# Optimization experiments

Hardware: AMD Instinct MI355X
Metric: run time of the kernel (lower is better)

Reference implementation:

```python
import jax, jax.numpy as jnp
import numpy as np

HID = 2048 * 3  # infl_ratio = 3
EPS = 1e-5
P_DROP = 0.5


def sign_ste(x):
    # straight-through binarization: sign in fwd, identity in bwd
    return x + jax.lax.stop_gradient(jnp.sign(x) - x)


def batchnorm(x, g, b):
    # training-mode BatchNorm1d: batch stats, biased variance
    m = jnp.mean(x, axis=0)
    v = jnp.mean((x - m) ** 2, axis=0)
    return g * (x - m) / jnp.sqrt(v + EPS) + b


def hardtanh(x):
    return jnp.clip(x, -1.0, 1.0)


def dropout(x, u):
    # u ~ U[0,1); keep where u >= p, scale by 1/(1-p)
    return jnp.where(u >= P_DROP, x / (1.0 - P_DROP), 0.0)


def setup_inputs() -> dict:
    key = jax.random.key(0)
    ks = jax.random.split(key, 16)
    B = 512
    d = {}
    d['x'] = jax.random.normal(ks[0], (B, 784), dtype=jnp.float32)
    d['drop_mask_bin'] = jax.random.uniform(ks[1], (B, HID), dtype=jnp.float32)
    d['drop_mask_real'] = jax.random.uniform(ks[2], (B, HID), dtype=jnp.float32)
    s1 = 1.0 / np.sqrt(784)
    sh = 1.0 / np.sqrt(HID)
    d['w1'] = jax.random.uniform(ks[3], (HID, 784), jnp.float32, -s1, s1)
    d['b1'] = jax.random.uniform(ks[4], (HID,), jnp.float32, -s1, s1)
    d['w2'] = jax.random.uniform(ks[5], (HID, HID), jnp.float32, -sh, sh)
    d['b2'] = jax.random.uniform(ks[6], (HID,), jnp.float32, -sh, sh)
    d['w3'] = jax.random.uniform(ks[7], (HID, HID), jnp.float32, -sh, sh)
    d['b3'] = jax.random.uniform(ks[8], (HID,), jnp.float32, -sh, sh)
    d['w4'] = jax.random.uniform(ks[9], (10, HID), jnp.float32, -sh, sh)
    d['b4'] = jax.random.uniform(ks[10], (10,), jnp.float32, -sh, sh)
    for i, k in zip((1, 2, 3), (ks[11], ks[12], ks[13])):
        d[f'g{i}'] = jnp.ones((HID,), jnp.float32)
        d[f'be{i}'] = jnp.zeros((HID,), jnp.float32)
    return d


def reference(x, drop_mask_bin, drop_mask_real, w1, b1, w2, b2, w3, b3, w4, b4,
              g1, be1, g2, be2, g3, be3):
    sg = jax.lax.stop_gradient
    # layer 1: input dim 784 -> input NOT binarized; weights binarized
    Bout1 = x @ sign_ste(w1).T + b1
    Rout1 = sg(x @ w1.T + b1)
    Bout1 = hardtanh(batchnorm(Bout1, g1, be1))
    Rout1 = sg(hardtanh(batchnorm(Rout1, g1, be1)))
    # layer 2: binarize activations and weights on binary path
    Bout2 = sign_ste(Bout1) @ sign_ste(w2).T + b2
    Rout2 = sg(Rout1 @ w2.T + b2)
    Bout2 = hardtanh(batchnorm(Bout2, g2, be2))
    Rout2 = sg(hardtanh(batchnorm(Rout2, g2, be2)))
    # layer 3 + dropout
    Bout3 = sign_ste(Bout2) @ sign_ste(w3).T + b3
    Rout3 = sg(Rout2 @ w3.T + b3)
    Bout3 = hardtanh(batchnorm(dropout(Bout3, drop_mask_bin), g3, be3))
    Rout3 = sg(hardtanh(batchnorm(dropout(Rout3, drop_mask_real), g3, be3)))
    # classifier (real-valued Linear)
    out = Bout3 @ w4.T + b4
    logp = jax.nn.log_softmax(out, axis=1)
    return (logp, out, Bout1, Rout1, Bout2, Rout2, Bout3, Rout3)
```

## Files before the change

kernel.cpp:

```cpp
#include <hip/hip_runtime.h>


typedef _Float16 f16x8 __attribute__((ext_vector_type(8)));
typedef _Float16 f16x4 __attribute__((ext_vector_type(4)));
typedef float f32x4 __attribute__((ext_vector_type(4)));
typedef int i32x4 __attribute__((ext_vector_type(4)));

#define MFMA16(a, b, c) __builtin_amdgcn_mfma_f32_16x16x32_f16((a), (b), (c), 0, 0, 0)
#define MFMAI8K64(a, b, c) __builtin_amdgcn_mfma_i32_16x16x64_i8((a), (b), (c), 0, 0, 0)

#define HIDC 6144
#define BATCH 512

#define OFF_XH    0ull
#define OFF_A8S1  851968ull
#define OFF_SB8   13434880ull
#define OFF_RF    16580608ull
#define OFF_STATS 22872064ull
#define OFF_PPART 23068672ull
#define OFF_ZPB   24641536ull
#define OFF_ZPR   37224448ull
#define OFF_ZPR2  49807360ull
#define OFF_ZPR3  62390272ull
#define OFF_W1V   74973184ull
#define OFF_WV    85196800ull
#define OFF_WS8   160694272ull
#define WS_NEED   198443008ull

#define A8_STRIDE 458752ull

__device__ __forceinline__ void load_lds16(const void* g, char* lds) {
  __builtin_amdgcn_global_load_lds((const __attribute__((address_space(1))) void*)g,
                                   (__attribute__((address_space(3))) void*)lds, 16, 0, 0);
}

__global__ __launch_bounds__(256) void k_prep_all(const float* __restrict__ x,
                                                  const float* __restrict__ w,
                                                  char* __restrict__ a8,
                                                  _Float16* __restrict__ xh,
                                                  char* __restrict__ s1,
                                                  _Float16* __restrict__ w1v) {
  if (blockIdx.x < 1792) {
    int idx = blockIdx.x * 256 + threadIdx.x;
    if (idx >= 512 * 896) return;
    int row = idx / 896, k = idx - row * 896;
    float v = (k < 784) ? x[(size_t)row * 784 + k] : 0.f;
    int q = (int)lrintf(v * 16777216.0f);
    int d0 = ((q + 128) & 255) - 128; q = (q - d0) >> 8;
    int d1 = ((q + 128) & 255) - 128; q = (q - d1) >> 8;
    int d2 = ((q + 128) & 255) - 128; q = (q - d2) >> 8;
    a8[idx] = (char)d0;
    a8[A8_STRIDE + idx] = (char)d1;
    a8[2 * A8_STRIDE + idx] = (char)d2;
    a8[3 * A8_STRIDE + idx] = (char)q;
    if (k < 832) xh[(size_t)row * 832 + k] = (_Float16)v;
  } else {
    int idx = (blockIdx.x - 1792) * 256 + threadIdx.x;
    if (idx >= 6144 * 896) return;
    int r = idx / 896, k = idx - r * 896;
    float v = (k < 784) ? w[(size_t)r * 784 + k] : 0.f;
    s1[idx] = v > 0.f ? 1 : (v < 0.f ? -1 : 0);
    if (k < 832) w1v[(size_t)r * 832 + k] = (_Float16)v;
  }
}

__global__ __launch_bounds__(256) void k_conv_w23(const float* __restrict__ w,
                                                  _Float16* __restrict__ wv,
                                                  char* __restrict__ ws8) {
  int idx = blockIdx.x * 256 + threadIdx.x;
  size_t o8 = (size_t)idx * 8;
  const float* s = w + o8;
  float4 v0 = *(const float4*)s;
  float4 v1 = *(const float4*)(s + 4);
  float a[8] = {v0.x, v0.y, v0.z, v0.w, v1.x, v1.y, v1.z, v1.w};
  f16x8 hv;
  unsigned long long sbits = 0;
#pragma unroll
  for (int e = 0; e < 8; ++e) {
    hv[e] = (_Float16)a[e];
    char sg = a[e] > 0.f ? 1 : (a[e] < 0.f ? -1 : 0);
    sbits |= ((unsigned long long)(unsigned char)sg) << (8 * e);
  }
  *(f16x8*)(wv + o8) = hv;
  *(unsigned long long*)(ws8 + o8) = sbits;
}

struct MixJob {
  const void* A;
  const void* B;
  float* C;
  int K;
  int kstart;
  int ksteps;
  int is8;
};
struct Mix6 { MixJob j[6]; };

__global__ __launch_bounds__(256) void k_gemm_mix(Mix6 P) {
  __shared__ __align__(16) char smem[65536];
  MixJob J = P.j[0];
  if (blockIdx.z == 1) J = P.j[1];
  if (blockIdx.z == 2) J = P.j[2];
  if (blockIdx.z == 3) J = P.j[3];
  if (blockIdx.z == 4) J = P.j[4];
  if (blockIdx.z == 5) J = P.j[5];
  const int t = threadIdx.x;
  const int lane = t & 63, wid = t >> 6;
  const int wm = wid >> 1, wn = wid & 1;
  const int bn = blockIdx.x, bm = blockIdx.y;
  const size_t K = (size_t)J.K;
  const int nt = J.ksteps;

  if (J.is8) {
    const char* A = (const char*)J.A;
    const char* B = (const char*)J.B;
    i32x4 acc[4][4];
#pragma unroll
    for (int mf = 0; mf < 4; ++mf)
#pragma unroll
      for (int nf = 0; nf < 4; ++nf) acc[mf][nf] = (i32x4){0, 0, 0, 0};

    auto stage = [&](char* dst, int k0) {
#pragma unroll
      for (int i = 0; i < 4; ++i) {
        int p = i * 256 + t;
        int r = p >> 3, c = p & 7;
        int cs = c ^ (r & 7);
        load_lds16(A + (size_t)(bm * 128 + r) * K + k0 + cs * 16, dst + p * 16);
      }
#pragma unroll
      for (int i = 0; i < 4; ++i) {
        int p = i * 256 + t;
        int r = p >> 3, c = p & 7;
        int cs = c ^ (r & 7);
        load_lds16(B + (size_t)(bn * 128 + r) * K + k0 + cs * 16, dst + 16384 + p * 16);
      }
    };

    stage(smem, J.kstart);
    for (int kt = 0; kt < nt; ++kt) {
      char* cbuf = smem + (kt & 1) * 32768;
      char* nbuf = smem + ((kt + 1) & 1) * 32768;
      if (kt + 1 < nt) {
        stage(nbuf, J.kstart + (kt + 1) * 128);
        asm volatile("s_waitcnt vmcnt(8)" ::: "memory");
      } else {
        asm volatile("s_waitcnt vmcnt(0)" ::: "memory");
      }
      __builtin_amdgcn_s_barrier();
      __builtin_amdgcn_s_setprio(1);
#pragma unroll
      for (int kk = 0; kk < 2; ++kk) {
        i32x4 av[4], bv[4];
#pragma unroll
        for (int mf = 0; mf < 4; ++mf) {
          int r = wm * 64 + mf * 16 + (lane & 15);
          int bo = (r * 128 + kk * 64 + (lane >> 4) * 16) ^ ((r & 7) << 4);
          av[mf] = *(const i32x4*)(cbuf + bo);
        }
#pragma unroll
        for (int nf = 0; nf < 4; ++nf) {
          int r = wn * 64 + nf * 16 + (lane & 15);
          int bo = (r * 128 + kk * 64 + (lane >> 4) * 16) ^ ((r & 7) << 4);
          bv[nf] = *(const i32x4*)(cbuf + 16384 + bo);
        }
#pragma unroll
        for (int mf = 0; mf < 4; ++mf)
#pragma unroll
          for (int nf = 0; nf < 4; ++nf) acc[mf][nf] = MFMAI8K64(av[mf], bv[nf], acc[mf][nf]);
      }
      __builtin_amdgcn_s_setprio(0);
      __builtin_amdgcn_s_barrier();
    }
#pragma unroll
    for (int mf = 0; mf < 4; ++mf)
#pragma unroll
      for (int nf = 0; nf < 4; ++nf) {
        int col = bn * 128 + wn * 64 + nf * 16 + (lane & 15);
        int row0 = bm * 128 + wm * 64 + mf * 16 + ((lane >> 4) << 2);
#pragma unroll
        for (int rr = 0; rr < 4; ++rr) {
          J.C[(size_t)(row0 + rr) * HIDC + col] = (float)acc[mf][nf][rr];
        }
      }
  } else {
    const _Float16* A = (const _Float16*)J.A;
    const _Float16* B = (const _Float16*)J.B;
    f32x4 acc[4][4];
#pragma unroll
    for (int mf = 0; mf < 4; ++mf)
#pragma unroll
      for (int nf = 0; nf < 4; ++nf) acc[mf][nf] = (f32x4){0.f, 0.f, 0.f, 0.f};

    auto stage = [&](char* dst, int k0) {
#pragma unroll
      for (int i = 0; i < 4; ++i) {
        int p = i * 256 + t;
        int r = p >> 3, c = p & 7;
        int cs = c ^ (r & 7);
        load_lds16(A + (size_t)(bm * 128 + r) * K + k0 + cs * 8, dst + p * 16);
      }
#pragma unroll
      for (int i = 0; i < 4; ++i) {
        int p = i * 256 + t;
        int r = p >> 3, c = p & 7;
        int cs = c ^ (r & 7);
        load_lds16(B + (size_t)(bn * 128 + r) * K + k0 + cs * 8, dst + 16384 + p * 16);
      }
    };

    stage(smem, J.kstart);
    for (int kt = 0; kt < nt; ++kt) {
      char* cbuf = smem + (kt & 1) * 32768;
      char* nbuf = smem + ((kt + 1) & 1) * 32768;
      if (kt + 1 < nt) {
        stage(nbuf, J.kstart + (kt + 1) * 64);
        asm volatile("s_waitcnt vmcnt(8)" ::: "memory");
      } else {
        asm volatile("s_waitcnt vmcnt(0)" ::: "memory");
      }
      __builtin_amdgcn_s_barrier();
      __builtin_amdgcn_s_setprio(1);
#pragma unroll
      for (int kk = 0; kk < 2; ++kk) {
        f16x8 av[4], bv[4];
#pragma unroll
        for (int mf = 0; mf < 4; ++mf) {
          int r = wm * 64 + mf * 16 + (lane & 15);
          int bo = (r * 128 + kk * 64 + (lane >> 4) * 16) ^ ((r & 7) << 4);
          av[mf] = *(const f16x8*)(cbuf + bo);
        }
#pragma unroll
        for (int nf = 0; nf < 4; ++nf) {
          int r = wn * 64 + nf * 16 + (lane & 15);
          int bo = (r * 128 + kk * 64 + (lane >> 4) * 16) ^ ((r & 7) << 4);
          bv[nf] = *(const f16x8*)(cbuf + 16384 + bo);
        }
#pragma unroll
        for (int mf = 0; mf < 4; ++mf)
#pragma unroll
          for (int nf = 0; nf < 4; ++nf) acc[mf][nf] = MFMA16(av[mf], bv[nf], acc[mf][nf]);
      }
      __builtin_amdgcn_s_setprio(0);
      __builtin_amdgcn_s_barrier();
    }
#pragma unroll
    for (int mf = 0; mf < 4; ++mf)
#pragma unroll
      for (int nf = 0; nf < 4; ++nf) {
        int col = bn * 128 + wn * 64 + nf * 16 + (lane & 15);
        int row0 = bm * 128 + wm * 64 + mf * 16 + ((lane >> 4) << 2);
#pragma unroll
        for (int rr = 0; rr < 4; ++rr) {
          J.C[(size_t)(row0 + rr) * HIDC + col] = acc[mf][nf][rr];
        }
      }
  }
}

struct StJob { const float* Z; const float* Zp0; const float* Zp1; const float* Zp2;
               const float* msk; int digitmode; };
struct St2 { StJob j[2]; const float* bias; int dodrop; double* ppart; };

__global__ __launch_bounds__(256) void k_stats_part(St2 P) {
  __shared__ double sm[4][64];
  __shared__ double sq[4][64];
  const int z = blockIdx.z;
  StJob J = z ? P.j[1] : P.j[0];
  const int li = threadIdx.x & 63, rg = threadIdx.x >> 6;
  const int col = blockIdx.x * 64 + li;
  const double bb = P.dodrop ? (double)P.bias[col] : 0.0;
  double s = 0.0, s2 = 0.0;
#pragma unroll 4
  for (int rr = 0; rr < 16; ++rr) {
    int r = blockIdx.y * 64 + rg * 16 + rr;
    size_t i = (size_t)r * HIDC + col;
    double v;
    if (J.digitmode) {
      double d0 = (double)J.Z[i], d1 = (double)J.Zp0[i];
      double d2 = (double)J.Zp1[i], d3 = (double)J.Zp2[i];
      v = (((d3 * 256.0 + d2) * 256.0 + d1) * 256.0 + d0) * (1.0 / 16777216.0);
    } else {
      v = (double)J.Z[i];
      if (J.Zp0) v += (double)J.Zp0[i];
      if (J.Zp1) v += (double)J.Zp1[i];
      if (J.Zp2) v += (double)J.Zp2[i];
    }
    if (P.dodrop) v = (J.msk[i] >= 0.5f) ? 2.0 * (v + bb) : 0.0;
    s += v;
    s2 += v * v;
  }
  sm[rg][li] = s;
  sq[rg][li] = s2;
  __syncthreads();
  if (rg == 0) {
    double S = sm[0][li] + sm[1][li] + sm[2][li] + sm[3][li];
    double S2 = sq[0][li] + sq[1][li] + sq[2][li] + sq[3][li];
    size_t o = ((size_t)(z * 8 + blockIdx.y) * 2) * HIDC + col;
    P.ppart[o] = S;
    P.ppart[o + HIDC] = S2;
  }
}

__global__ __launch_bounds__(256) void k_stats_fin(const double* __restrict__ ppart,
                                                   double* __restrict__ stats) {
  const int z = blockIdx.z;
  const int c = blockIdx.x * 256 + threadIdx.x;
  double S = 0.0, S2 = 0.0;
#pragma unroll
  for (int y = 0; y < 8; ++y) {
    size_t o = ((size_t)(z * 8 + y) * 2) * HIDC + c;
    S += ppart[o];
    S2 += ppart[o + HIDC];
  }
  double m = S / 512.0;
  double var = S2 / 512.0 - m * m;
  stats[z * 2 * HIDC + c] = m;
  stats[z * 2 * HIDC + HIDC + c] = 1.0 / sqrt(var + 1e-5);
}

struct BnJob { float* Z; const float* Zp0; const float* Zp1; const float* Zp2;
               const float* Zp3; void* aux; const float* msk; int auxmode; int digitmode; };
struct Bn2 {
  BnJob j[2];
  const double* stats;
  const float* g; const float* be; const float* bias;
  int dodrop;
};

__global__ __launch_bounds__(256) void k_bn2(Bn2 P) {
  const int z = blockIdx.z;
  BnJob J = z ? P.j[1] : P.j[0];
  const double* m_arr = P.stats + (size_t)z * 2 * HIDC;
  const double* r_arr = m_arr + HIDC;
  int idx = blockIdx.x * 256 + threadIdx.x;
  int row = idx / 1536;
  int c4 = (idx - row * 1536) * 4;
  size_t base = (size_t)row * HIDC + c4;
  double vv[4];
  if (J.digitmode) {
    float4 d0 = *(const float4*)(J.Zp0 + base);
    float4 d1 = *(const float4*)(J.Zp1 + base);
    float4 d2 = *(const float4*)(J.Zp2 + base);
    float4 d3 = *(const float4*)(J.Zp3 + base);
    const float* p0 = &d0.x;
    const float* p1 = &d1.x;
    const float* p2 = &d2.x;
    const float* p3 = &d3.x;
#pragma unroll
    for (int e = 0; e < 4; ++e)
      vv[e] = ((((double)p3[e] * 256.0 + (double)p2[e]) * 256.0 + (double)p1[e]) * 256.0 +
               (double)p0[e]) * (1.0 / 16777216.0);
  } else {
    float4 zv = *(const float4*)(J.Z + base);
    vv[0] = zv.x; vv[1] = zv.y; vv[2] = zv.z; vv[3] = zv.w;
    if (J.Zp0) {
      float4 t4 = *(const float4*)(J.Zp0 + base);
      vv[0] += t4.x; vv[1] += t4.y; vv[2] += t4.z; vv[3] += t4.w;
    }
    if (J.Zp1) {
      float4 t4 = *(const float4*)(J.Zp1 + base);
      vv[0] += t4.x; vv[1] += t4.y; vv[2] += t4.z; vv[3] += t4.w;
    }
    if (J.Zp2) {
      float4 t4 = *(const float4*)(J.Zp2 + base);
      vv[0] += t4.x; vv[1] += t4.y; vv[2] += t4.z; vv[3] += t4.w;
    }
  }
  float mk[4] = {1.f, 1.f, 1.f, 1.f};
  if (P.dodrop) {
    float4 t4 = *(const float4*)(J.msk + base);
    mk[0] = t4.x; mk[1] = t4.y; mk[2] = t4.z; mk[3] = t4.w;
  }
  float o[4];
  f16x4 a4;
  int sbits = 0;
#pragma unroll
  for (int e = 0; e < 4; ++e) {
    int c = c4 + e;
    double v = vv[e];
    if (P.dodrop) v = (mk[e] >= 0.5f) ? 2.0 * (v + (double)P.bias[c]) : 0.0;
    double bnv = (double)P.g[c] * ((v - m_arr[c]) * r_arr[c]) + (double)P.be[c];
    bnv = bnv > 1.0 ? 1.0 : (bnv < -1.0 ? -1.0 : bnv);
    o[e] = (float)bnv;
    char sg = bnv > 0.0 ? 1 : (bnv < 0.0 ? -1 : 0);
    sbits |= ((int)(unsigned char)sg) << (8 * e);
    a4[e] = (_Float16)o[e];
  }
  float4 ov = {o[0], o[1], o[2], o[3]};
  *(float4*)(J.Z + base) = ov;
  if (J.auxmode == 0) *(int*)((char*)J.aux + base) = sbits;
  if (J.auxmode == 1) *(f16x4*)((_Float16*)J.aux + base) = a4;
}

__global__ __launch_bounds__(256) void k_head(const float* __restrict__ B3,
                                              const float* __restrict__ w4,
                                              const float* __restrict__ b4,
                                              float* __restrict__ out,
                                              float* __restrict__ logp) {
  const int row = blockIdx.x, t = threadIdx.x;
  float acc[10];
#pragma unroll
  for (int j = 0; j < 10; ++j) acc[j] = 0.f;
  const float* a = B3 + (size_t)row * HIDC;
  for (int k4 = t; k4 < 1536; k4 += 256) {
    float4 av = *(const float4*)(a + k4 * 4);
#pragma unroll
    for (int j = 0; j < 10; ++j) {
      float4 wv = *(const float4*)(w4 + (size_t)j * HIDC + k4 * 4);
      acc[j] += av.x * wv.x + av.y * wv.y + av.z * wv.z + av.w * wv.w;
    }
  }
#pragma unroll
  for (int j = 0; j < 10; ++j)
    for (int off = 32; off; off >>= 1) acc[j] += __shfl_down(acc[j], off);
  __shared__ float sred[4][10];
  int wid = t >> 6, ln = t & 63;
  if (ln == 0)
#pragma unroll
    for (int j = 0; j < 10; ++j) sred[wid][j] = acc[j];
  __syncthreads();
  if (t == 0) {
    double o[10];
    double mx = -1e300;
#pragma unroll
    for (int j = 0; j < 10; ++j) {
      o[j] = (double)sred[0][j] + sred[1][j] + sred[2][j] + sred[3][j] + (double)b4[j];
      mx = o[j] > mx ? o[j] : mx;
    }
    double s = 0.0;
#pragma unroll
    for (int j = 0; j < 10; ++j) s += exp(o[j] - mx);
    double l = log(s) + mx;
#pragma unroll
    for (int j = 0; j < 10; ++j) {
      out[row * 10 + j] = (float)o[j];
      logp[row * 10 + j] = (float)(o[j] - l);
    }
  }
}

extern "C" void kernel_launch(void* const* d_in, const int* in_sizes, int n_in,
                              void* d_out, int out_size, void* d_ws, size_t ws_size,
                              hipStream_t stream) {
  const float* x   = (const float*)d_in[0];
  const float* mkb = (const float*)d_in[1];
  const float* mkr = (const float*)d_in[2];
  const float* w1  = (const float*)d_in[3];
  const float* w2  = (const float*)d_in[5];
  const float* w3  = (const float*)d_in[7];
  const float* b3  = (const float*)d_in[8];
  const float* w4  = (const float*)d_in[9];
  const float* b4  = (const float*)d_in[10];
  const float* g1  = (const float*)d_in[11]; const float* be1 = (const float*)d_in[12];
  const float* g2  = (const float*)d_in[13]; const float* be2 = (const float*)d_in[14];
  const float* g3  = (const float*)d_in[15]; const float* be3 = (const float*)d_in[16];

  float* outp = (float*)d_out;
  float* logp = outp;
  float* outo = outp + 5120;
  float* B1 = outp + 10240;
  float* R1 = outp + 3155968;
  float* B2 = outp + 6301696;
  float* R2 = outp + 9447424;
  float* B3 = outp + 12593152;
  float* R3 = outp + 15738880;

  char* ws = (char*)d_ws;
  _Float16* xh  = (_Float16*)(ws + OFF_XH);
  char* a8      = (char*)(ws + OFF_A8S1);
  char* s1      = (char*)(ws + OFF_A8S1 + 4ull * A8_STRIDE);
  char* sB8     = (char*)(ws + OFF_SB8);
  _Float16* rF  = (_Float16*)(ws + OFF_RF);
  double* stats = (double*)(ws + OFF_STATS);
  double* ppart = (double*)(ws + OFF_PPART);
  float* zpb    = (float*)(ws + OFF_ZPB);
  float* zpr    = (float*)(ws + OFF_ZPR);
  float* zpr2   = (float*)(ws + OFF_ZPR2);
  float* zpr3   = (float*)(ws + OFF_ZPR3);
  _Float16* w1v = (_Float16*)(ws + OFF_W1V);
  _Float16* wv  = (_Float16*)(ws + OFF_WV);
  char* ws8     = (char*)(ws + OFF_WS8);

  k_prep_all<<<23296, 256, 0, stream>>>(x, w1, a8, xh, s1, w1v);
  {
    Mix6 P{};
    P.j[0] = {a8,                 s1, zpb,  896, 0, 7, 1};
    P.j[1] = {a8 + A8_STRIDE,     s1, zpr,  896, 0, 7, 1};
    P.j[2] = {a8 + 2 * A8_STRIDE, s1, zpr2, 896, 0, 7, 1};
    P.j[3] = {a8 + 3 * A8_STRIDE, s1, zpr3, 896, 0, 7, 1};
    P.j[4] = {xh, w1v, R1, 832, 0, 13, 0};
    P.j[5] = P.j[4];
    k_gemm_mix<<<dim3(48, 4, 5), 256, 0, stream>>>(P);
  }
  {
    St2 S{};
    S.j[0] = {zpb, zpr, zpr2, zpr3, nullptr, 1};
    S.j[1] = {R1, nullptr, nullptr, nullptr, nullptr, 0};
    S.bias = nullptr; S.dodrop = 0; S.ppart = ppart;
    k_stats_part<<<dim3(96, 8, 2), 256, 0, stream>>>(S);
    k_stats_fin<<<dim3(24, 1, 2), 256, 0, stream>>>(ppart, stats);
    Bn2 B{};
    B.j[0] = {B1, zpb, zpr, zpr2, zpr3, sB8, nullptr, 0, 1};
    B.j[1] = {R1, nullptr, nullptr, nullptr, nullptr, rF, nullptr, 1, 0};
    B.stats = stats; B.g = g1; B.be = be1; B.bias = nullptr; B.dodrop = 0;
    k_bn2<<<dim3(3072, 1, 2), 256, 0, stream>>>(B);
  }
  k_conv_w23<<<18432, 256, 0, stream>>>(w2, wv, ws8);
  {
    Mix6 P{};
    P.j[0] = {sB8, ws8, B2,  HIDC, 0,    24, 1};
    P.j[1] = {sB8, ws8, zpb, HIDC, 3072, 24, 1};
    P.j[2] = {rF,  wv,  R2,  HIDC, 0,    48, 0};
    P.j[3] = {rF,  wv,  zpr, HIDC, 3072, 48, 0};
    k_gemm_mix<<<dim3(48, 4, 4), 256, 0, stream>>>(P);
  }
  {
    St2 S{};
    S.j[0] = {B2, zpb, nullptr, nullptr, nullptr, 0};
    S.j[1] = {R2, zpr, nullptr, nullptr, nullptr, 0};
    S.bias = nullptr; S.dodrop = 0; S.ppart = ppart;
    k_stats_part<<<dim3(96, 8, 2), 256, 0, stream>>>(S);
    k_stats_fin<<<dim3(24, 1, 2), 256, 0, stream>>>(ppart, stats);
    Bn2 B{};
    B.j[0] = {B2, zpb, nullptr, nullptr, nullptr, sB8, nullptr, 0, 0};
    B.j[1] = {R2, zpr, nullptr, nullptr, nullptr, rF, nullptr, 1, 0};
    B.stats = stats; B.g = g2; B.be = be2; B.bias = nullptr; B.dodrop = 0;
    k_bn2<<<dim3(3072, 1, 2), 256, 0, stream>>>(B);
  }
  k_conv_w23<<<18432, 256, 0, stream>>>(w3, wv, ws8);
  {
    Mix6 P{};
    P.j[0] = {sB8, ws8, B3,  HIDC, 0,    24, 1};
    P.j[1] = {sB8, ws8, zpb, HIDC, 3072, 24, 1};
    P.j[2] = {rF,  wv,  R3,  HIDC, 0,    48, 0};
    P.j[3] = {rF,  wv,  zpr, HIDC, 3072, 48, 0};
    k_gemm_mix<<<dim3(48, 4, 4), 256, 0, stream>>>(P);
  }
  {
    St2 S{};
    S.j[0] = {B3, zpb, nullptr, nullptr, mkb, 0};
    S.j[1] = {R3, zpr, nullptr, nullptr, mkr, 0};
    S.bias = b3; S.dodrop = 1; S.ppart = ppart;
    k_stats_part<<<dim3(96, 8, 2), 256, 0, stream>>>(S);
    k_stats_fin<<<dim3(24, 1, 2), 256, 0, stream>>>(ppart, stats);
    Bn2 B{};
    B.j[0] = {B3, zpb, nullptr, nullptr, nullptr, nullptr, mkb, 2, 0};
    B.j[1] = {R3, zpr, nullptr, nullptr, nullptr, nullptr, mkr, 2, 0};
    B.stats = stats; B.g = g3; B.be = be3; B.bias = b3; B.dodrop = 1;
    k_bn2<<<dim3(3072, 1, 2), 256, 0, stream>>>(B);
  }
  k_head<<<512, 256, 0, stream>>>(B3, w4, b4, outo, logp);
}
```

Before: 454.3 us.

## Fuse BatchNorm column statistics into GEMM epilogue and drop split-K for layers 2-3

Layers 2 and 3 no longer split K into two halves with partial outputs. Each GEMM block now covers the full K range and writes the final output directly. Its epilogue also accumulates per-column sum and sum-of-squares in double, applying the dropout mask and bias for layer 3, reduces them across waves through LDS and writes per-block partials. A small finalize kernel combines the four row-block partials, which removes the separate stats pass, its re-read of the GEMM outputs, and the split-K partial reads and writes. The trade-off is a grid halved to 384 blocks with twice-longer K loops, which lowers parallelism, plus extra epilogue work and mask loads inside the GEMM.

```diff
diff --git a/kernel.cpp b/kernel.cpp
--- a/kernel.cpp
+++ b/kernel.cpp
@@ -89,12 +89,16 @@
   const void* A;
   const void* B;
   float* C;
+  const float* msk;
+  const float* bias;
   int K;
   int kstart;
   int ksteps;
   int is8;
+  int slot;
+  int dodrop;
 };
-struct Mix6 { MixJob j[6]; };
+struct Mix6 { MixJob j[6]; double* ppart; };
 
 __global__ __launch_bounds__(256) void k_gemm_mix(Mix6 P) {
   __shared__ __align__(16) char smem[65536];
@@ -111,6 +115,10 @@
   const size_t K = (size_t)J.K;
   const int nt = J.ksteps;
 
+  double s[4], s2[4];
+#pragma unroll
+  for (int nf = 0; nf < 4; ++nf) { s[nf] = 0.0; s2[nf] = 0.0; }
+
   if (J.is8) {
     const char* A = (const char*)J.A;
     const char* B = (const char*)J.B;
@@ -183,6 +191,25 @@
           J.C[(size_t)(row0 + rr) * HIDC + col] = (float)acc[mf][nf][rr];
         }
       }
+    if (J.slot >= 0) {
+#pragma unroll
+      for (int mf = 0; mf < 4; ++mf)
+#pragma unroll
+        for (int nf = 0; nf < 4; ++nf) {
+          int col = bn * 128 + wn * 64 + nf * 16 + (lane & 15);
+          int row0 = bm * 128 + wm * 64 + mf * 16 + ((lane >> 4) << 2);
+#pragma unroll
+          for (int rr = 0; rr < 4; ++rr) {
+            double v = (double)acc[mf][nf][rr];
+            if (J.dodrop) {
+              float mv = J.msk[(size_t)(row0 + rr) * HIDC + col];
+              v = (mv >= 0.5f) ? 2.0 * (v + (double)J.bias[col]) : 0.0;
+            }
+            s[nf] += v;
+            s2[nf] += v * v;
+          }
+        }
+    }
   } else {
     const _Float16* A = (const _Float16*)J.A;
     const _Float16* B = (const _Float16*)J.B;
@@ -255,6 +282,60 @@
           J.C[(size_t)(row0 + rr) * HIDC + col] = acc[mf][nf][rr];
         }
       }
+    if (J.slot >= 0) {
+#pragma unroll
+      for (int mf = 0; mf < 4; ++mf)
+#pragma unroll
+        for (int nf = 0; nf < 4; ++nf) {
+          int col = bn * 128 + wn * 64 + nf * 16 + (lane & 15);
+          int row0 = bm * 128 + wm * 64 + mf * 16 + ((lane >> 4) << 2);
+#pragma unroll
+          for (int rr = 0; rr < 4; ++rr) {
+            double v = (double)acc[mf][nf][rr];
+            if (J.dodrop) {
+              float mv = J.msk[(size_t)(row0 + rr) * HIDC + col];
+              v = (mv >= 0.5f) ? 2.0 * (v + (double)J.bias[col]) : 0.0;
+            }
+            s[nf] += v;
+            s2[nf] += v * v;
+          }
+        }
+    }
+  }
+
+  if (J.slot >= 0) {
+#pragma unroll
+    for (int nf = 0; nf < 4; ++nf) {
+      s[nf] += __shfl_xor(s[nf], 16);
+      s[nf] += __shfl_xor(s[nf], 32);
+      s2[nf] += __shfl_xor(s2[nf], 16);
+      s2[nf] += __shfl_xor(s2[nf], 32);
+    }
+    __syncthreads();
+    double* sred = (double*)smem;
+    if ((lane >> 4) == 0) {
+#pragma unroll
+      for (int nf = 0; nf < 4; ++nf) {
+        int ix = (((wm * 2 + wn) * 4 + nf) * 16 + (lane & 15)) * 2;
+        sred[ix] = s[nf];
+        sred[ix + 1] = s2[nf];
+      }
+    }
+    __syncthreads();
+    if (wm == 0 && (lane >> 4) == 0) {
+#pragma unroll
+      for (int nf = 0; nf < 4; ++nf) {
+        int l = lane & 15;
+        int i0 = (((0 * 2 + wn) * 4 + nf) * 16 + l) * 2;
+        int i1 = (((1 * 2 + wn) * 4 + nf) * 16 + l) * 2;
+        double S = sred[i0] + sred[i1];
+        double S2 = sred[i0 + 1] + sred[i1 + 1];
+        int col = bn * 128 + wn * 64 + nf * 16 + l;
+        size_t o = ((size_t)(J.slot * 4 + bm) * 2) * HIDC + col;
+        P.ppart[o] = S;
+        P.ppart[o + HIDC] = S2;
+      }
+    }
   }
 }
 
@@ -319,6 +400,23 @@
   stats[z * 2 * HIDC + HIDC + c] = 1.0 / sqrt(var + 1e-5);
 }
 
+__global__ __launch_bounds__(256) void k_stats_fin4(const double* __restrict__ ppart,
+                                                    double* __restrict__ stats) {
+  const int z = blockIdx.z;
+  const int c = blockIdx.x * 256 + threadIdx.x;
+  double S = 0.0, S2 = 0.0;
+#pragma unroll
+  for (int b = 0; b < 4; ++b) {
+    size_t o = ((size_t)(z * 4 + b) * 2) * HIDC + c;
+    S += ppart[o];
+    S2 += ppart[o + HIDC];
+  }
+  double m = S / 512.0;
+  double var = S2 / 512.0 - m * m;
+  stats[z * 2 * HIDC + c] = m;
+  stats[z * 2 * HIDC + HIDC + c] = 1.0 / sqrt(var + 1e-5);
+}
+
 struct BnJob { float* Z; const float* Zp0; const float* Zp1; const float* Zp2;
                const float* Zp3; void* aux; const float* msk; int auxmode; int digitmode; };
 struct Bn2 {
@@ -358,14 +456,6 @@
       float4 t4 = *(const float4*)(J.Zp0 + base);
       vv[0] += t4.x; vv[1] += t4.y; vv[2] += t4.z; vv[3] += t4.w;
     }
-    if (J.Zp1) {
-      float4 t4 = *(const float4*)(J.Zp1 + base);
-      vv[0] += t4.x; vv[1] += t4.y; vv[2] += t4.z; vv[3] += t4.w;
-    }
-    if (J.Zp2) {
-      float4 t4 = *(const float4*)(J.Zp2 + base);
-      vv[0] += t4.x; vv[1] += t4.y; vv[2] += t4.z; vv[3] += t4.w;
-    }
   }
   float mk[4] = {1.f, 1.f, 1.f, 1.f};
   if (P.dodrop) {
@@ -485,12 +575,13 @@
   k_prep_all<<<23296, 256, 0, stream>>>(x, w1, a8, xh, s1, w1v);
   {
     Mix6 P{};
-    P.j[0] = {a8,                 s1, zpb,  896, 0, 7, 1};
-    P.j[1] = {a8 + A8_STRIDE,     s1, zpr,  896, 0, 7, 1};
-    P.j[2] = {a8 + 2 * A8_STRIDE, s1, zpr2, 896, 0, 7, 1};
-    P.j[3] = {a8 + 3 * A8_STRIDE, s1, zpr3, 896, 0, 7, 1};
-    P.j[4] = {xh, w1v, R1, 832, 0, 13, 0};
+    P.j[0] = {a8,                 s1, zpb,  nullptr, nullptr, 896, 0, 7, 1, -1, 0};
+    P.j[1] = {a8 + A8_STRIDE,     s1, zpr,  nullptr, nullptr, 896, 0, 7, 1, -1, 0};
+    P.j[2] = {a8 + 2 * A8_STRIDE, s1, zpr2, nullptr, nullptr, 896, 0, 7, 1, -1, 0};
+    P.j[3] = {a8 + 3 * A8_STRIDE, s1, zpr3, nullptr, nullptr, 896, 0, 7, 1, -1, 0};
+    P.j[4] = {xh, w1v, R1, nullptr, nullptr, 832, 0, 13, 0, -1, 0};
     P.j[5] = P.j[4];
+    P.ppart = ppart;
     k_gemm_mix<<<dim3(48, 4, 5), 256, 0, stream>>>(P);
   }
   {
@@ -509,44 +600,34 @@
   k_conv_w23<<<18432, 256, 0, stream>>>(w2, wv, ws8);
   {
     Mix6 P{};
-    P.j[0] = {sB8, ws8, B2,  HIDC, 0,    24, 1};
-    P.j[1] = {sB8, ws8, zpb, HIDC, 3072, 24, 1};
-    P.j[2] = {rF,  wv,  R2,  HIDC, 0,    48, 0};
-    P.j[3] = {rF,  wv,  zpr, HIDC, 3072, 48, 0};
-    k_gemm_mix<<<dim3(48, 4, 4), 256, 0, stream>>>(P);
+    P.j[0] = {sB8, ws8, B2, nullptr, nullptr, HIDC, 0, 48, 1, 0, 0};
+    P.j[1] = {rF,  wv,  R2, nullptr, nullptr, HIDC, 0, 96, 0, 1, 0};
+    P.j[2] = P.j[0]; P.j[3] = P.j[0]; P.j[4] = P.j[0]; P.j[5] = P.j[0];
+    P.ppart = ppart;
+    k_gemm_mix<<<dim3(48, 4, 2), 256, 0, stream>>>(P);
   }
   {
-    St2 S{};
-    S.j[0] = {B2, zpb, nullptr, nullptr, nullptr, 0};
-    S.j[1] = {R2, zpr, nullptr, nullptr, nullptr, 0};
-    S.bias = nullptr; S.dodrop = 0; S.ppart = ppart;
-    k_stats_part<<<dim3(96, 8, 2), 256, 0, stream>>>(S);
-    k_stats_fin<<<dim3(24, 1, 2), 256, 0, stream>>>(ppart, stats);
+    k_stats_fin4<<<dim3(24, 1, 2), 256, 0, stream>>>(ppart, stats);
     Bn2 B{};
-    B.j[0] = {B2, zpb, nullptr, nullptr, nullptr, sB8, nullptr, 0, 0};
-    B.j[1] = {R2, zpr, nullptr, nullptr, nullptr, rF, nullptr, 1, 0};
+    B.j[0] = {B2, nullptr, nullptr, nullptr, nullptr, sB8, nullptr, 0, 0};
+    B.j[1] = {R2, nullptr, nullptr, nullptr, nullptr, rF, nullptr, 1, 0};
     B.stats = stats; B.g = g2; B.be = be2; B.bias = nullptr; B.dodrop = 0;
     k_bn2<<<dim3(3072, 1, 2), 256, 0, stream>>>(B);
   }
   k_conv_w23<<<18432, 256, 0, stream>>>(w3, wv, ws8);
   {
     Mix6 P{};
-    P.j[0] = {sB8, ws8, B3,  HIDC, 0,    24, 1};
-    P.j[1] = {sB8, ws8, zpb, HIDC, 3072, 24, 1};
-    P.j[2] = {rF,  wv,  R3,  HIDC, 0,    48, 0};
-    P.j[3] = {rF,  wv,  zpr, HIDC, 3072, 48, 0};
-    k_gemm_mix<<<dim3(48, 4, 4), 256, 0, stream>>>(P);
+    P.j[0] = {sB8, ws8, B3, mkb, b3, HIDC, 0, 48, 1, 0, 1};
+    P.j[1] = {rF,  wv,  R3, mkr, b3, HIDC, 0, 96, 0, 1, 1};
+    P.j[2] = P.j[0]; P.j[3] = P.j[0]; P.j[4] = P.j[0]; P.j[5] = P.j[0];
+    P.ppart = ppart;
+    k_gemm_mix<<<dim3(48, 4, 2), 256, 0, stream>>>(P);
   }
   {
-    St2 S{};
-    S.j[0] = {B3, zpb, nullptr, nullptr, mkb, 0};
-    S.j[1] = {R3, zpr, nullptr, nullptr, mkr, 0};
-    S.bias = b3; S.dodrop = 1; S.ppart = ppart;
-    k_stats_part<<<dim3(96, 8, 2), 256, 0, stream>>>(S);
-    k_stats_fin<<<dim3(24, 1, 2), 256, 0, stream>>>(ppart, stats);
+    k_stats_fin4<<<dim3(24, 1, 2), 256, 0, stream>>>(ppart, stats);
     Bn2 B{};
-    B.j[0] = {B3, zpb, nullptr, nullptr, nullptr, nullptr, mkb, 2, 0};
-    B.j[1] = {R3, zpr, nullptr, nullptr, nullptr, nullptr, mkr, 2, 0};
+    B.j[0] = {B3, nullptr, nullptr, nullptr, nullptr, nullptr, mkb, 2, 0};
+    B.j[1] = {R3, nullptr, nullptr, nullptr, nullptr, nullptr, mkr, 2, 0};
     B.stats = stats; B.g = g3; B.be = be3; B.bias = b3; B.dodrop = 1;
     k_bn2<<<dim3(3072, 1, 2), 256, 0, stream>>>(B);
   }
```

Result: no change. 460.0 us (+1.3%).
